# Performance work log

Measured on AMD Instinct MI355X. Metric: run time of the kernel, lower is better.

## Reference

```python
import jax, jax.numpy as jnp
import numpy as np

ALPHA = 0.2        # LeakyReLU negative slope (config['alpha'])
NEG_INF = -9e15    # mask value from the original code


def setup_inputs() -> dict:
    key = jax.random.key(0)
    k1, k2, k3, k4 = jax.random.split(key, 4)
    N, Fin, Fout = 8192, 512, 256
    inp = jax.random.normal(k1, (N, Fin), dtype=jnp.float32)
    adj = jax.random.randint(k2, (N, N), 0, 2, dtype=jnp.int32)
    # xavier_uniform with gain=1.414
    limW = 1.414 * np.sqrt(6.0 / (Fin + Fout))
    W = jax.random.uniform(k3, (Fin, Fout), dtype=jnp.float32, minval=-limW, maxval=limW)
    lima = 1.414 * np.sqrt(6.0 / (2 * Fout + 1))
    a = jax.random.uniform(k4, (2 * Fout, 1), dtype=jnp.float32, minval=-lima, maxval=lima)
    return {"input": inp, "adj": adj, "W": W, "a": a}


def reference(input, adj, W, a):
    # h: [N, F]
    h = input @ W
    Fout = W.shape[1]
    # The original builds a_input[i, j] = concat(h_i, h_j) and dots with a.
    # Equivalently: e_ij = leakyrelu(h_i . a[:F] + h_j . a[F:]), computed
    # without the O(N^2 * 2F) intermediate.
    s1 = h @ a[:Fout, 0]   # [N] contribution from node i
    s2 = h @ a[Fout:, 0]   # [N] contribution from node j
    e = s1[:, None] + s2[None, :]                     # [N, N]
    e = jnp.where(e > 0, e, ALPHA * e)                # LeakyReLU
    scores = jnp.where(adj > 0, e, NEG_INF)
    attention = jax.nn.softmax(scores, axis=1)        # row-wise softmax
    # dropout is identity in inference mode (training=False)
    h_prime = attention @ h                           # [N, F]
    return jax.nn.elu(h_prime)                        # concat=True path
```

## Files before the change

kernel.cpp:

```cpp
#include <hip/hip_runtime.h>
#include <stdint.h>
#include <stddef.h>


#define N_NODES 8192
#define FIN     512
#define FOUT    256
#define LRALPHA 0.2f
#define MI_SHIFT 16.0f

typedef float f32x4 __attribute__((ext_vector_type(4)));
typedef short s16x8 __attribute__((ext_vector_type(8)));
typedef unsigned short u16x4 __attribute__((ext_vector_type(4)));
typedef int   i32x4 __attribute__((ext_vector_type(4)));
typedef unsigned long long u64;

__device__ __forceinline__ short f2bf_rne(float f) {
  uint32_t u = __builtin_bit_cast(uint32_t, f);
  u += 0x7fffu + ((u >> 16) & 1u);
  return (short)(u >> 16);
}
__device__ __forceinline__ short f2bf_fast(float f) {
  uint32_t u = __builtin_bit_cast(uint32_t, f);
  return (short)((u + 0x8000u) >> 16);
}
__device__ __forceinline__ float bf2f(short s) {
  uint32_t u = ((uint32_t)(uint16_t)s) << 16;
  return __builtin_bit_cast(float, u);
}

__global__ __launch_bounds__(256) void k_prep(const float* __restrict__ W,
                                              uint16_t* __restrict__ WThi,
                                              uint16_t* __restrict__ WTlo) {
  const int idx = blockIdx.x * 256 + threadIdx.x;
  const int n = idx >> 9;
  const int k = idx & 511;
  float v = W[k * FOUT + n];
  short h = f2bf_rne(v);
  WThi[idx] = (uint16_t)h;
  WTlo[idx] = (uint16_t)f2bf_rne(v - bf2f(h));
}

__global__ __launch_bounds__(256, 4) void k_gemm(const float* __restrict__ X,
                                                 const uint16_t* __restrict__ WThi,
                                                 const uint16_t* __restrict__ WTlo,
                                                 const float* __restrict__ a,
                                                 uint16_t* __restrict__ HTf,
                                                 float* __restrict__ s1g,
                                                 float* __restrict__ s2g) {
  __shared__ float ls1[16], ls2[16];
  __shared__ uint16_t tile[FOUT * 16];
  const int lane = threadIdx.x & 63;
  const int w    = threadIdx.x >> 6;
  const int m    = lane & 15;
  const int quad = lane >> 4;
  const int i0   = blockIdx.x * 16;
  const int colg = w * 64;

  f32x4 acc[4];
#pragma unroll
  for (int cb = 0; cb < 4; ++cb) { f32x4 z = {0.f,0.f,0.f,0.f}; acc[cb] = z; }

  for (int kt = 0; kt < FIN / 32; ++kt) {
    const int k0 = kt * 32 + quad * 8;
    const float* ap = X + (size_t)(i0 + m) * FIN + k0;
    f32x4 a0 = *(const f32x4*)ap;
    f32x4 a1 = *(const f32x4*)(ap + 4);
    s16x8 ahi, alo;
#pragma unroll
    for (int e = 0; e < 4; ++e) {
      short h0 = f2bf_rne(a0[e]); ahi[e] = h0; alo[e] = f2bf_rne(a0[e] - bf2f(h0));
      short h1 = f2bf_rne(a1[e]); ahi[4+e] = h1; alo[4+e] = f2bf_rne(a1[e] - bf2f(h1));
    }
#pragma unroll
    for (int cb = 0; cb < 4; ++cb) {
      const int n = colg + cb * 16 + m;
      s16x8 bhi = *(const s16x8*)(WThi + (size_t)n * FIN + k0);
      s16x8 blo = *(const s16x8*)(WTlo + (size_t)n * FIN + k0);
      acc[cb] = __builtin_amdgcn_mfma_f32_16x16x32_bf16(ahi, bhi, acc[cb], 0, 0, 0);
      acc[cb] = __builtin_amdgcn_mfma_f32_16x16x32_bf16(ahi, blo, acc[cb], 0, 0, 0);
      acc[cb] = __builtin_amdgcn_mfma_f32_16x16x32_bf16(alo, bhi, acc[cb], 0, 0, 0);
    }
  }

  float p1[4] = {0.f,0.f,0.f,0.f}, p2[4] = {0.f,0.f,0.f,0.f};
#pragma unroll
  for (int cb = 0; cb < 4; ++cb) {
    const int n = colg + cb * 16 + m;
    const float a1c = a[n];
    const float a2c = a[FOUT + n];
#pragma unroll
    for (int reg = 0; reg < 4; ++reg) {
      p1[reg] += acc[cb][reg] * a1c;
      p2[reg] += acc[cb][reg] * a2c;
    }
  }
#pragma unroll
  for (int off = 1; off <= 8; off <<= 1)
#pragma unroll
    for (int reg = 0; reg < 4; ++reg) {
      p1[reg] += __shfl_xor(p1[reg], off);
      p2[reg] += __shfl_xor(p2[reg], off);
    }
  if (threadIdx.x < 16) { ls1[threadIdx.x] = 0.f; ls2[threadIdx.x] = 0.f; }
  __syncthreads();
  if (m == 0) {
#pragma unroll
    for (int reg = 0; reg < 4; ++reg) {
      atomicAdd(&ls1[quad * 4 + reg], p1[reg]);
      atomicAdd(&ls2[quad * 4 + reg], p2[reg]);
    }
  }
#pragma unroll
  for (int cb = 0; cb < 4; ++cb) {
    const int col = colg + cb * 16 + m;
    u16x4 pk;
#pragma unroll
    for (int reg = 0; reg < 4; ++reg) pk[reg] = (uint16_t)f2bf_rne(acc[cb][reg]);
    *(u16x4*)(tile + col * 16 + quad * 4) = pk;
  }
  __syncthreads();
  const int t = threadIdx.x;
  if (t < 16) { s1g[i0 + t] = ls1[t]; s2g[i0 + t] = ls2[t]; }
  const int jt = i0 >> 5;
  const int qh = (i0 >> 4) & 1;
  const int c  = t >> 4;
  const int mm = t & 15;
#pragma unroll
  for (int qq = 0; qq < 2; ++qq) {
    uint4 v = *(const uint4*)(tile + (c * 16 + mm) * 16 + qq * 8);
    *(uint4*)(HTf + ((((size_t)jt * 16 + c) * 64) + (qh * 2 + qq) * 16 + mm) * 8) = v;
  }
}

__global__ __launch_bounds__(512, 4) void k_attn(const int* __restrict__ adj,
                                                 const uint16_t* __restrict__ HTf,
                                                 const float* __restrict__ s1,
                                                 const float* __restrict__ s2,
                                                 float* __restrict__ pout,
                                                 float* __restrict__ pden,
                                                 int split) {
  __shared__ uint16_t PL[2][4096];
  __shared__ float lss2[1024];

  const int tid  = threadIdx.x;
  const int lane = tid & 63;
  const int w    = tid >> 6;
  const int m    = lane & 15;
  const int q    = lane >> 4;
  const int rg   = w >> 2, cg = w & 3;
  const int pr   = tid >> 2;
  const int cpr  = tid & 3;
  const int i0   = blockIdx.x * 128;
  const int sp   = blockIdx.y;
  const int jrange = N_NODES / split;
  const int jbeg   = sp * jrange;
  const int nphase = jrange / 32;

  const float s1r = s1[i0 + pr];
  const float mi = fmaxf(s1r + MI_SHIFT, LRALPHA * (s1r + MI_SHIFT));

  f32x4 acc[4][4];
#pragma unroll
  for (int rt = 0; rt < 4; ++rt)
#pragma unroll
    for (int cb = 0; cb < 4; ++cb) { f32x4 z = {0.f,0.f,0.f,0.f}; acc[rt][cb] = z; }
  float den = 0.f;

  const int* arow = adj + (size_t)(i0 + pr) * N_NODES + jbeg + cpr * 8;
  i32x4 A0 = *(const i32x4*)arow;
  i32x4 A1 = *(const i32x4*)(arow + 4);

#pragma unroll 1
  for (int p = 0; p < nphase; ++p) {
    if ((p & 31) == 0) {
      __syncthreads();
      if (tid < 256) *(f32x4*)(lss2 + tid * 4) =
        *(const f32x4*)(s2 + jbeg + (p >> 5) * 1024 + tid * 4);
      __syncthreads();
    }
    const int pn = (p + 1 < nphase) ? p + 1 : p;
    i32x4 nA0 = *(const i32x4*)(arow + pn * 32);
    i32x4 nA1 = *(const i32x4*)(arow + pn * 32 + 4);
    const int pl = p & 31;
    f32x4 sA = *(const f32x4*)(lss2 + pl * 32 + cpr * 8);
    f32x4 sB = *(const f32x4*)(lss2 + pl * 32 + cpr * 8 + 4);
    s16x8 P0;
#pragma unroll
    for (int e = 0; e < 4; ++e) {
      float x0 = s1r + sA[e];
      float pv0 = __expf(fmaxf(x0, LRALPHA * x0) - mi);
      pv0 = (A0[e] != 0) ? pv0 : 0.f;
      den += pv0; P0[e] = f2bf_fast(pv0);
      float x1 = s1r + sB[e];
      float pv1 = __expf(fmaxf(x1, LRALPHA * x1) - mi);
      pv1 = (A1[e] != 0) ? pv1 : 0.f;
      den += pv1; P0[4 + e] = f2bf_fast(pv1);
    }
    *(s16x8*)(PL[p & 1] + (cpr * 128 + pr) * 8) = P0;
    A0 = nA0; A1 = nA1;
    __syncthreads();
    const uint16_t* hB = HTf + ((size_t)((jbeg >> 5) + p) * 16 + cg * 4) * 512 + lane * 8;
    s16x8 Bv[4];
#pragma unroll
    for (int cb = 0; cb < 4; ++cb)
      Bv[cb] = *(const s16x8*)(hB + cb * 512);
    s16x8 F[4];
#pragma unroll
    for (int rt = 0; rt < 4; ++rt)
      F[rt] = *(const s16x8*)(PL[p & 1] + (q * 128 + rg * 64 + rt * 16 + m) * 8);
#pragma unroll
    for (int rt = 0; rt < 4; ++rt)
#pragma unroll
      for (int cb = 0; cb < 4; ++cb)
        acc[rt][cb] = __builtin_amdgcn_mfma_f32_16x16x32_bf16(F[rt], Bv[cb], acc[rt][cb], 0, 0, 0);
  }

  den += __shfl_xor(den, 1);
  den += __shfl_xor(den, 2);
  if (cpr == 0) pden[(size_t)sp * N_NODES + i0 + pr] = den;
#pragma unroll
  for (int rt = 0; rt < 4; ++rt)
#pragma unroll
    for (int cb = 0; cb < 4; ++cb)
#pragma unroll
      for (int reg = 0; reg < 4; ++reg) {
        const int row = i0 + rg * 64 + rt * 16 + q * 4 + reg;
        const int col = cg * 64 + cb * 16 + m;
        pout[((size_t)sp * N_NODES + row) * FOUT + col] = acc[rt][cb][reg];
      }
}

__global__ __launch_bounds__(256) void k_reduce(const float* __restrict__ pout,
                                                const float* __restrict__ pden,
                                                float* __restrict__ out,
                                                int split) {
  const int gid = blockIdx.x * 256 + threadIdx.x;
  const int i = gid >> 6;
  const int c = (gid & 63) << 2;
  f32x4 sum = {0.f,0.f,0.f,0.f};
  float den = 0.f;
  for (int s = 0; s < split; ++s) {
    sum += *(const f32x4*)(pout + ((size_t)s * N_NODES + i) * FOUT + c);
    den += pden[(size_t)s * N_NODES + i];
  }
  const float inv = 1.0f / den;
  f32x4 r;
#pragma unroll
  for (int e = 0; e < 4; ++e) {
    float v = sum[e] * inv;
    r[e] = v > 0.f ? v : (__expf(v) - 1.0f);
  }
  *(f32x4*)(out + (size_t)i * FOUT + c) = r;
}

extern "C" void kernel_launch(void* const* d_in, const int* in_sizes, int n_in,
                              void* d_out, int out_size, void* d_ws, size_t ws_size,
                              hipStream_t stream) {
  const float* X   = (const float*)d_in[0];
  const int*   adj = (const int*)d_in[1];
  const float* W   = (const float*)d_in[2];
  const float* a   = (const float*)d_in[3];
  float* out = (float*)d_out;

  char* ws = (char*)d_ws;
  uint16_t* HTf  = (uint16_t*)ws;
  uint16_t* WThi = (uint16_t*)(ws + (4u << 20));
  uint16_t* WTlo = (uint16_t*)(ws + (4u << 20) + 262144);
  float*    s1   = (float*)(ws + (4u << 20) + 524288);
  float*    s2   = s1 + N_NODES;
  float*    pden = s2 + N_NODES;
  const size_t pout_off = (size_t)16u << 20;
  const size_t slab = (size_t)N_NODES * FOUT * sizeof(float);

  int split;
  if      (ws_size >= pout_off + 8 * slab) split = 8;
  else if (ws_size >= pout_off + 4 * slab) split = 4;
  else if (ws_size >= pout_off + 2 * slab) split = 2;
  else                                     split = 1;
  float* pout = (split == 1) ? out : (float*)(ws + pout_off);

  k_prep<<<dim3(512), dim3(256), 0, stream>>>(W, WThi, WTlo);
  k_gemm<<<dim3(N_NODES / 16), dim3(256), 0, stream>>>(X, WThi, WTlo, a, HTf, s1, s2);
  k_attn<<<dim3(N_NODES / 128, split), dim3(512), 0, stream>>>(adj, HTf, s1, s2, pout, pden, split);
  k_reduce<<<dim3(N_NODES * FOUT / 4 / 256), dim3(256), 0, stream>>>(pout, pden, out, split);
}
```

Measured before the change: 481.0 us.

## Double attention block to 1024 threads with padded P tile and deeper adj prefetch

Raises the attention kernel from 512 to 1024 threads per block, so each thread handles 4 adjacency entries per phase instead of 8 and each wave owns 2 row tiles instead of 4. The shared P tile becomes row-major with a padded stride of 40 to avoid bank conflicts. Adjacency loads are prefetched two phases ahead, and the HTf B-operand load is issued before the exp work to hide its latency. Fewer accumulators per thread lower register pressure, but each block now reloads the B fragments for half as many rows per wave and synchronises more threads per barrier.

```diff
diff --git a/kernel.cpp b/kernel.cpp
--- a/kernel.cpp
+++ b/kernel.cpp
@@ -133,14 +133,14 @@
   }
 }
 
-__global__ __launch_bounds__(512, 4) void k_attn(const int* __restrict__ adj,
-                                                 const uint16_t* __restrict__ HTf,
-                                                 const float* __restrict__ s1,
-                                                 const float* __restrict__ s2,
-                                                 float* __restrict__ pout,
-                                                 float* __restrict__ pden,
-                                                 int split) {
-  __shared__ uint16_t PL[2][4096];
+__global__ __launch_bounds__(1024, 4) void k_attn(const int* __restrict__ adj,
+                                                  const uint16_t* __restrict__ HTf,
+                                                  const float* __restrict__ s1,
+                                                  const float* __restrict__ s2,
+                                                  float* __restrict__ pout,
+                                                  float* __restrict__ pden,
+                                                  int split) {
+  __shared__ uint16_t PL[2][128 * 40];
   __shared__ float lss2[1024];
 
   const int tid  = threadIdx.x;
@@ -149,8 +149,8 @@
   const int m    = lane & 15;
   const int q    = lane >> 4;
   const int rg   = w >> 2, cg = w & 3;
-  const int pr   = tid >> 2;
-  const int cpr  = tid & 3;
+  const int pr   = tid >> 3;
+  const int cpr  = tid & 7;
   const int i0   = blockIdx.x * 128;
   const int sp   = blockIdx.y;
   const int jrange = N_NODES / split;
@@ -160,16 +160,16 @@
   const float s1r = s1[i0 + pr];
   const float mi = fmaxf(s1r + MI_SHIFT, LRALPHA * (s1r + MI_SHIFT));
 
-  f32x4 acc[4][4];
-#pragma unroll
-  for (int rt = 0; rt < 4; ++rt)
+  f32x4 acc[2][4];
+#pragma unroll
+  for (int rt = 0; rt < 2; ++rt)
 #pragma unroll
     for (int cb = 0; cb < 4; ++cb) { f32x4 z = {0.f,0.f,0.f,0.f}; acc[rt][cb] = z; }
   float den = 0.f;
 
-  const int* arow = adj + (size_t)(i0 + pr) * N_NODES + jbeg + cpr * 8;
-  i32x4 A0 = *(const i32x4*)arow;
-  i32x4 A1 = *(const i32x4*)(arow + 4);
+  const int* arow = adj + (size_t)(i0 + pr) * N_NODES + jbeg + cpr * 4;
+  i32x4 A_cur = *(const i32x4*)arow;
+  i32x4 A_nxt = *(const i32x4*)(arow + ((1 < nphase) ? 32 : 0));
 
 #pragma unroll 1
   for (int p = 0; p < nphase; ++p) {
@@ -179,38 +179,33 @@
         *(const f32x4*)(s2 + jbeg + (p >> 5) * 1024 + tid * 4);
       __syncthreads();
     }
-    const int pn = (p + 1 < nphase) ? p + 1 : p;
-    i32x4 nA0 = *(const i32x4*)(arow + pn * 32);
-    i32x4 nA1 = *(const i32x4*)(arow + pn * 32 + 4);
-    const int pl = p & 31;
-    f32x4 sA = *(const f32x4*)(lss2 + pl * 32 + cpr * 8);
-    f32x4 sB = *(const f32x4*)(lss2 + pl * 32 + cpr * 8 + 4);
-    s16x8 P0;
-#pragma unroll
-    for (int e = 0; e < 4; ++e) {
-      float x0 = s1r + sA[e];
-      float pv0 = __expf(fmaxf(x0, LRALPHA * x0) - mi);
-      pv0 = (A0[e] != 0) ? pv0 : 0.f;
-      den += pv0; P0[e] = f2bf_fast(pv0);
-      float x1 = s1r + sB[e];
-      float pv1 = __expf(fmaxf(x1, LRALPHA * x1) - mi);
-      pv1 = (A1[e] != 0) ? pv1 : 0.f;
-      den += pv1; P0[4 + e] = f2bf_fast(pv1);
-    }
-    *(s16x8*)(PL[p & 1] + (cpr * 128 + pr) * 8) = P0;
-    A0 = nA0; A1 = nA1;
-    __syncthreads();
     const uint16_t* hB = HTf + ((size_t)((jbeg >> 5) + p) * 16 + cg * 4) * 512 + lane * 8;
     s16x8 Bv[4];
 #pragma unroll
     for (int cb = 0; cb < 4; ++cb)
       Bv[cb] = *(const s16x8*)(hB + cb * 512);
-    s16x8 F[4];
-#pragma unroll
-    for (int rt = 0; rt < 4; ++rt)
-      F[rt] = *(const s16x8*)(PL[p & 1] + (q * 128 + rg * 64 + rt * 16 + m) * 8);
-#pragma unroll
-    for (int rt = 0; rt < 4; ++rt)
+    const int pn = (p + 2 < nphase) ? p + 2 : p;
+    i32x4 A_pf = *(const i32x4*)(arow + pn * 32);
+    const int pl = p & 31;
+    f32x4 sA = *(const f32x4*)(lss2 + pl * 32 + cpr * 4);
+    u16x4 P0;
+#pragma unroll
+    for (int e = 0; e < 4; ++e) {
+      float x = s1r + sA[e];
+      float pv = __expf(fmaxf(x, LRALPHA * x) - mi);
+      pv = (A_cur[e] != 0) ? pv : 0.f;
+      den += pv;
+      P0[e] = (uint16_t)f2bf_fast(pv);
+    }
+    *(u16x4*)(PL[p & 1] + pr * 40 + cpr * 4) = P0;
+    A_cur = A_nxt; A_nxt = A_pf;
+    __syncthreads();
+    s16x8 F[2];
+#pragma unroll
+    for (int rt = 0; rt < 2; ++rt)
+      F[rt] = *(const s16x8*)(PL[p & 1] + (rg * 32 + rt * 16 + m) * 40 + q * 8);
+#pragma unroll
+    for (int rt = 0; rt < 2; ++rt)
 #pragma unroll
       for (int cb = 0; cb < 4; ++cb)
         acc[rt][cb] = __builtin_amdgcn_mfma_f32_16x16x32_bf16(F[rt], Bv[cb], acc[rt][cb], 0, 0, 0);
@@ -218,14 +213,15 @@
 
   den += __shfl_xor(den, 1);
   den += __shfl_xor(den, 2);
+  den += __shfl_xor(den, 4);
   if (cpr == 0) pden[(size_t)sp * N_NODES + i0 + pr] = den;
 #pragma unroll
-  for (int rt = 0; rt < 4; ++rt)
+  for (int rt = 0; rt < 2; ++rt)
 #pragma unroll
     for (int cb = 0; cb < 4; ++cb)
 #pragma unroll
       for (int reg = 0; reg < 4; ++reg) {
-        const int row = i0 + rg * 64 + rt * 16 + q * 4 + reg;
+        const int row = i0 + rg * 32 + rt * 16 + q * 4 + reg;
         const int col = cg * 64 + cb * 16 + m;
         pout[((size_t)sp * N_NODES + row) * FOUT + col] = acc[rt][cb][reg];
       }
@@ -282,6 +278,6 @@
 
   k_prep<<<dim3(512), dim3(256), 0, stream>>>(W, WThi, WTlo);
   k_gemm<<<dim3(N_NODES / 16), dim3(256), 0, stream>>>(X, WThi, WTlo, a, HTf, s1, s2);
-  k_attn<<<dim3(N_NODES / 128, split), dim3(512), 0, stream>>>(adj, HTf, s1, s2, pout, pden, split);
+  k_attn<<<dim3(N_NODES / 128, split), dim3(1024), 0, stream>>>(adj, HTf, s1, s2, pout, pden, split);
   k_reduce<<<dim3(N_NODES * FOUT / 4 / 256), dim3(256), 0, stream>>>(pout, pden, out, split);
 }
```

New measurement: 499.7 us. 1.04x slower.
